# Performance work log

Measured on AMD Instinct MI355X. Metric: run time of the kernel, lower is better.

The kernel has to match this reference:

```python
import jax, jax.numpy as jnp
import numpy as np

B, S, D = 2, 2048, 4096
H, KVH, HD = 32, 8, 128   # attention heads, kv heads, head_dim
GROUPS = H // KVH          # 4
SCALING = 0.08838834764831845  # attention_multiplier = 1/sqrt(head_dim)
NEG = -1e9


def _rope_tables(seq_len, head_dim, base=10000.0):
    half = head_dim // 2
    inv_freq = 1.0 / (base ** (np.arange(0, half, dtype=np.float32) / half))
    t = np.arange(seq_len, dtype=np.float32)
    freqs = np.outer(t, inv_freq)               # [S, half]
    emb = np.concatenate([freqs, freqs], axis=-1)  # [S, head_dim]
    return jnp.asarray(np.cos(emb)), jnp.asarray(np.sin(emb))


def setup_inputs() -> dict:
    key = jax.random.key(0)
    ks = jax.random.split(key, 6)
    hidden_states = jax.random.normal(ks[0], (B, S, D), dtype=jnp.float32)
    std = 0.02
    Wq = jax.random.normal(ks[1], (D, H * HD), dtype=jnp.float32) * std
    Wk = jax.random.normal(ks[2], (D, KVH * HD), dtype=jnp.float32) * std
    Wv = jax.random.normal(ks[3], (D, KVH * HD), dtype=jnp.float32) * std
    Wo = jax.random.normal(ks[4], (H * HD, D), dtype=jnp.float32) * std
    cos1, sin1 = _rope_tables(S, HD)
    cos = jnp.broadcast_to(cos1[None], (B, S, HD))
    sin = jnp.broadcast_to(sin1[None], (B, S, HD))
    # additive causal mask [B, 1, S, S]
    causal = jnp.where(jnp.tril(jnp.ones((S, S), dtype=bool)), 0.0, NEG).astype(jnp.float32)
    attention_mask = jnp.broadcast_to(causal[None, None], (B, 1, S, S))
    return {"hidden_states": hidden_states, "cos": cos, "sin": sin,
            "attention_mask": attention_mask, "Wq": Wq, "Wk": Wk, "Wv": Wv, "Wo": Wo}


def _rotate_half(x):
    x1, x2 = jnp.split(x, 2, axis=-1)
    return jnp.concatenate([-x2, x1], axis=-1)


def reference(hidden_states, cos, sin, attention_mask, Wq, Wk, Wv, Wo):
    b, s, _ = hidden_states.shape
    # projections (no bias), split into heads: [B, H, S, HD]
    q = jnp.einsum('bsd,de->bse', hidden_states, Wq).reshape(b, s, H, HD).transpose(0, 2, 1, 3)
    k = jnp.einsum('bsd,de->bse', hidden_states, Wk).reshape(b, s, KVH, HD).transpose(0, 2, 1, 3)
    v = jnp.einsum('bsd,de->bse', hidden_states, Wv).reshape(b, s, KVH, HD).transpose(0, 2, 1, 3)
    # RoPE (cos/sin unsqueezed on head dim)
    c = cos[:, None, :, :]
    sn = sin[:, None, :, :]
    q = q * c + _rotate_half(q) * sn
    k = k * c + _rotate_half(k) * sn
    # repeat_kv: [B, KVH, S, HD] -> [B, H, S, HD]
    k = jnp.repeat(k, GROUPS, axis=1)
    v = jnp.repeat(v, GROUPS, axis=1)
    # eager attention: full score matrix, additive mask, fp32 softmax
    scores = jnp.einsum('bhqd,bhkd->bhqk', q, k) * SCALING + attention_mask
    attn_weights = jax.nn.softmax(scores.astype(jnp.float32), axis=-1).astype(q.dtype)
    attn_output = jnp.einsum('bhqk,bhkd->bhqd', attn_weights, v)
    attn_output = attn_output.transpose(0, 2, 1, 3).reshape(b, s, H * HD)
    attn_output = jnp.einsum('bse,ed->bsd', attn_output, Wo)
    return attn_output, attn_weights
```

## Files before the change

kernel.cpp:

```cpp
#include <hip/hip_runtime.h>

typedef unsigned short u16;
typedef unsigned int u32;
typedef __attribute__((ext_vector_type(8))) short bf16x8;
typedef __attribute__((ext_vector_type(4))) float f32x4;

#define SCALING 0.08838834764831845f

__device__ __forceinline__ float bf2f(u16 u) {
  union { u32 i; float f; } v; v.i = ((u32)u) << 16; return v.f;
}
__device__ __forceinline__ u16 f2bf(float f) {
  union { float f; u32 i; } v; v.f = f;
  u32 x = v.i;
  return (u16)((x + 0x7fffu + ((x >> 16) & 1u)) >> 16);
}

__device__ __forceinline__ void gll16(const void* g, void* l) {
  __builtin_amdgcn_global_load_lds((const __attribute__((address_space(1))) void*)g,
                                   (__attribute__((address_space(3))) void*)l, 16, 0, 0);
}

__global__ void cast_f32_to_bf16(const float* __restrict__ in, u16* __restrict__ out, int n4) {
  int i = blockIdx.x * 256 + threadIdx.x;
  if (i >= n4) return;
  float4 v = ((const float4*)in)[i];
  ushort4 o;
  o.x = f2bf(v.x); o.y = f2bf(v.y); o.z = f2bf(v.z); o.w = f2bf(v.w);
  ((ushort4*)out)[i] = o;
}

__global__ void transpose_cast(const float* __restrict__ W, u16* __restrict__ WT, int Kd, int Nd) {
  __shared__ float tile[32][33];
  int n0 = blockIdx.x * 32, k0 = blockIdx.y * 32;
  int t = threadIdx.x;
  int r = t >> 3;
  int c = (t & 7) * 4;
  float4 v = *(const float4*)(W + (size_t)(k0 + r) * Nd + n0 + c);
  tile[r][c + 0] = v.x; tile[r][c + 1] = v.y; tile[r][c + 2] = v.z; tile[r][c + 3] = v.w;
  __syncthreads();
  ushort4 o;
  o.x = f2bf(tile[c + 0][r]); o.y = f2bf(tile[c + 1][r]);
  o.z = f2bf(tile[c + 2][r]); o.w = f2bf(tile[c + 3][r]);
  *(ushort4*)(WT + (size_t)(n0 + r) * Kd + k0 + c) = o;
}

template <bool OUT_F32>
__global__ __launch_bounds__(256) void gemm_bt(const u16* __restrict__ A, const u16* __restrict__ B,
                                               void* __restrict__ C, int M, int N, int K) {
  __shared__ __align__(16) u16 As[128 * 32];
  __shared__ __align__(16) u16 Bs[128 * 32];
  const int tid = threadIdx.x;
  const int lane = tid & 63;
  const int w = tid >> 6;
  const int wr = w >> 1, wc = w & 1;
  const int q = lane >> 4, cl = lane & 15;
  const int m0 = blockIdx.y * 128, n0 = blockIdx.x * 128;

  const int srow = w * 16 + (lane >> 2);
  const int schk = (lane & 3) * 8;
  const u16* Ag0 = A + (size_t)(m0 + srow) * K + schk;
  const u16* Ag1 = Ag0 + (size_t)64 * K;
  const u16* Bg0 = B + (size_t)(n0 + srow) * K + schk;
  const u16* Bg1 = Bg0 + (size_t)64 * K;
  u16* Asp = As + srow * 32 + schk;
  u16* Bsp = Bs + srow * 32 + schk;

  f32x4 zero4 = {0.f, 0.f, 0.f, 0.f};
  f32x4 acc[4][4];
#pragma unroll
  for (int mi = 0; mi < 4; ++mi)
#pragma unroll
    for (int ni = 0; ni < 4; ++ni) acc[mi][ni] = zero4;

  for (int kk = 0; kk < K; kk += 32) {
    gll16(Ag0 + kk, Asp);
    gll16(Ag1 + kk, Asp + 64 * 32);
    gll16(Bg0 + kk, Bsp);
    gll16(Bg1 + kk, Bsp + 64 * 32);
    __syncthreads();
    bf16x8 af[4], bfv[4];
#pragma unroll
    for (int mi = 0; mi < 4; ++mi)
      af[mi] = *(const bf16x8*)(As + (wr * 64 + mi * 16 + cl) * 32 + q * 8);
#pragma unroll
    for (int ni = 0; ni < 4; ++ni)
      bfv[ni] = *(const bf16x8*)(Bs + (wc * 64 + ni * 16 + cl) * 32 + q * 8);
#pragma unroll
    for (int mi = 0; mi < 4; ++mi)
#pragma unroll
      for (int ni = 0; ni < 4; ++ni)
        acc[mi][ni] = __builtin_amdgcn_mfma_f32_16x16x32_bf16(af[mi], bfv[ni], acc[mi][ni], 0, 0, 0);
    __syncthreads();
  }

#pragma unroll
  for (int mi = 0; mi < 4; ++mi)
#pragma unroll
    for (int ni = 0; ni < 4; ++ni) {
      int row = m0 + wr * 64 + mi * 16 + q * 4;
      int col = n0 + wc * 64 + ni * 16 + cl;
#pragma unroll
      for (int r = 0; r < 4; ++r) {
        if (OUT_F32)
          ((float*)C)[(size_t)(row + r) * N + col] = acc[mi][ni][r];
        else
          ((u16*)C)[(size_t)(row + r) * N + col] = f2bf(acc[mi][ni][r]);
      }
    }
}

__global__ void rope_kernel(u16* __restrict__ X, const float* __restrict__ cosb,
                            const float* __restrict__ sinb, int rowstride) {
  int row = blockIdx.x;
  int v = blockIdx.y * 256 + threadIdx.x;
  int d = v & 63, hh = v >> 6;
  size_t base = (size_t)row * rowstride + hh * 128 + d;
  float x1 = bf2f(X[base]);
  float x2 = bf2f(X[base + 64]);
  const float* cp = cosb + (size_t)row * 128;
  const float* sp = sinb + (size_t)row * 128;
  X[base]      = f2bf(x1 * cp[d]      - x2 * sp[d]);
  X[base + 64] = f2bf(x2 * cp[d + 64] + x1 * sp[d + 64]);
}

__global__ __launch_bounds__(256, 2) void attn_kernel(
    const u16* __restrict__ Qb, const u16* __restrict__ Kb, const u16* __restrict__ Vb,
    float* __restrict__ Wout, u16* __restrict__ AO) {
  const int qt = blockIdx.x;
  const int h = blockIdx.y;
  const int b = blockIdx.z;
  const int kvh = h >> 2;

  __shared__ __align__(16) u16 KV[128 * 136];
  __shared__ __align__(16) u16 Ps[128 * 136];
  __shared__ float l_lds[128];
  __shared__ float r_lds[128];

  const int tid = threadIdx.x;
  const int lane = tid & 63;
  const int w = tid >> 6;
  const int wr = w >> 1, wc = w & 1;
  const int q = lane >> 4, cl = lane & 15;

  const size_t qrow0 = (size_t)b * 2048 + qt * 128;
  const u16* Qh = Qb + qrow0 * 4096 + h * 128;
  const u16* Kh = Kb + ((size_t)b * 2048) * 1024 + kvh * 128;
  const u16* Vh = Vb + ((size_t)b * 2048) * 1024 + kvh * 128;

  bf16x8 qa[4][4];
#pragma unroll
  for (int mi = 0; mi < 4; ++mi) {
    const u16* qp = Qh + (size_t)(wr * 64 + mi * 16 + cl) * 4096 + q * 8;
#pragma unroll
    for (int kd = 0; kd < 4; ++kd) qa[mi][kd] = *(const bf16x8*)(qp + kd * 32);
  }

  if (tid < 128) l_lds[tid] = 0.f;

  const int njt = qt + 1;
  const int srb = tid >> 4;
  const int scc = (tid & 15) * 8;

  f32x4 zero4 = {0.f, 0.f, 0.f, 0.f};

  for (int jt = 0; jt < njt; ++jt) {
    {
      const u16* src = Kh + (size_t)jt * 128 * 1024;
#pragma unroll
      for (int i = 0; i < 8; ++i) {
        int row = srb + i * 16;
        *(uint4*)(KV + row * 136 + scc) = *(const uint4*)(src + (size_t)row * 1024 + scc);
      }
    }
    __syncthreads();
    f32x4 acc[4][4];
#pragma unroll
    for (int mi = 0; mi < 4; ++mi)
#pragma unroll
      for (int ni = 0; ni < 4; ++ni) acc[mi][ni] = zero4;
#pragma unroll
    for (int kd = 0; kd < 4; ++kd) {
      bf16x8 bk[4];
#pragma unroll
      for (int ni = 0; ni < 4; ++ni)
        bk[ni] = *(const bf16x8*)(KV + (wc * 64 + ni * 16 + cl) * 136 + kd * 32 + q * 8);
#pragma unroll
      for (int mi = 0; mi < 4; ++mi)
#pragma unroll
        for (int ni = 0; ni < 4; ++ni)
          acc[mi][ni] = __builtin_amdgcn_mfma_f32_16x16x32_bf16(qa[mi][kd], bk[ni], acc[mi][ni], 0, 0, 0);
    }
#pragma unroll
    for (int mi = 0; mi < 4; ++mi) {
      int ig0 = qt * 128 + wr * 64 + mi * 16 + q * 4;
      float rs0 = 0.f, rs1 = 0.f, rs2 = 0.f, rs3 = 0.f;
#pragma unroll
      for (int ni = 0; ni < 4; ++ni) {
        int jg = jt * 128 + wc * 64 + ni * 16 + cl;
        rs0 += (jg <= ig0 + 0) ? __expf(acc[mi][ni][0] * SCALING) : 0.f;
        rs1 += (jg <= ig0 + 1) ? __expf(acc[mi][ni][1] * SCALING) : 0.f;
        rs2 += (jg <= ig0 + 2) ? __expf(acc[mi][ni][2] * SCALING) : 0.f;
        rs3 += (jg <= ig0 + 3) ? __expf(acc[mi][ni][3] * SCALING) : 0.f;
      }
#pragma unroll
      for (int m = 1; m < 16; m <<= 1) {
        rs0 += __shfl_xor(rs0, m, 64);
        rs1 += __shfl_xor(rs1, m, 64);
        rs2 += __shfl_xor(rs2, m, 64);
        rs3 += __shfl_xor(rs3, m, 64);
      }
      if (cl == 0) {
        int il = wr * 64 + mi * 16 + q * 4;
        atomicAdd(&l_lds[il + 0], rs0);
        atomicAdd(&l_lds[il + 1], rs1);
        atomicAdd(&l_lds[il + 2], rs2);
        atomicAdd(&l_lds[il + 3], rs3);
      }
    }
    __syncthreads();
  }
  if (tid < 128) r_lds[tid] = 1.f / l_lds[tid];

  f32x4 oacc[4][4];
#pragma unroll
  for (int mi = 0; mi < 4; ++mi)
#pragma unroll
    for (int ni = 0; ni < 4; ++ni) oacc[mi][ni] = zero4;
  __syncthreads();

  for (int jt = 0; jt < njt; ++jt) {
    {
      const u16* src = Kh + (size_t)jt * 128 * 1024;
#pragma unroll
      for (int i = 0; i < 8; ++i) {
        int row = srb + i * 16;
        *(uint4*)(KV + row * 136 + scc) = *(const uint4*)(src + (size_t)row * 1024 + scc);
      }
    }
    __syncthreads();
    f32x4 acc[4][4];
#pragma unroll
    for (int mi = 0; mi < 4; ++mi)
#pragma unroll
      for (int ni = 0; ni < 4; ++ni) acc[mi][ni] = zero4;
#pragma unroll
    for (int kd = 0; kd < 4; ++kd) {
      bf16x8 bk[4];
#pragma unroll
      for (int ni = 0; ni < 4; ++ni)
        bk[ni] = *(const bf16x8*)(KV + (wc * 64 + ni * 16 + cl) * 136 + kd * 32 + q * 8);
#pragma unroll
      for (int mi = 0; mi < 4; ++mi)
#pragma unroll
        for (int ni = 0; ni < 4; ++ni)
          acc[mi][ni] = __builtin_amdgcn_mfma_f32_16x16x32_bf16(qa[mi][kd], bk[ni], acc[mi][ni], 0, 0, 0);
    }
    __syncthreads();

    {
      const u16* src = Vh + (size_t)jt * 128 * 1024;
      u32* vt = (u32*)KV;
      int c = tid & 15;
      int d0 = c * 8;
#pragma unroll
      for (int i = 0; i < 4; ++i) {
        int jp = srb + i * 16;
        uint4 a = *(const uint4*)(src + (size_t)(2 * jp) * 1024 + d0);
        uint4 bq = *(const uint4*)(src + (size_t)(2 * jp + 1) * 1024 + d0);
        const u16* ah = (const u16*)&a;
        const u16* bh = (const u16*)&bq;
#pragma unroll
        for (int kk = 0; kk < 8; ++kk) {
          int k = (kk + c) & 7;
          vt[(d0 + k) * 68 + jp] = (u32)ah[k] | ((u32)bh[k] << 16);
        }
      }
    }
#pragma unroll
    for (int mi = 0; mi < 4; ++mi)
#pragma unroll
      for (int r = 0; r < 4; ++r) {
        int il = wr * 64 + mi * 16 + q * 4 + r;
        int ig = qt * 128 + il;
        float rv = r_lds[il];
#pragma unroll
        for (int ni = 0; ni < 4; ++ni) {
          int jl = wc * 64 + ni * 16 + cl;
          int jg = jt * 128 + jl;
          float p = (jg <= ig) ? __expf(acc[mi][ni][r] * SCALING) * rv : 0.f;
          Ps[il * 136 + jl] = f2bf(p);
        }
      }
    __syncthreads();

    {
      float* wb = Wout + ((size_t)(b * 32 + h) * 2048 + qt * 128) * 2048 + jt * 128;
#pragma unroll
      for (int i = 0; i < 8; ++i) {
        int cf = tid + i * 256;
        int row = cf >> 4;
        int ch = (cf & 15) * 8;
        const u16* sp = Ps + row * 136 + ch;
        float4 o0 = {bf2f(sp[0]), bf2f(sp[1]), bf2f(sp[2]), bf2f(sp[3])};
        float4 o1 = {bf2f(sp[4]), bf2f(sp[5]), bf2f(sp[6]), bf2f(sp[7])};
        float* dp = wb + (size_t)row * 2048 + ch;
        *(float4*)dp = o0;
        *(float4*)(dp + 4) = o1;
      }
    }
    {
      const u32* vt = (const u32*)KV;
#pragma unroll
      for (int ks = 0; ks < 4; ++ks) {
        bf16x8 pa[4], vb[4];
#pragma unroll
        for (int mi = 0; mi < 4; ++mi)
          pa[mi] = *(const bf16x8*)(Ps + (wr * 64 + mi * 16 + cl) * 136 + ks * 32 + q * 8);
#pragma unroll
        for (int ni = 0; ni < 4; ++ni)
          vb[ni] = *(const bf16x8*)(vt + (wc * 64 + ni * 16 + cl) * 68 + ks * 16 + q * 4);
#pragma unroll
        for (int mi = 0; mi < 4; ++mi)
#pragma unroll
          for (int ni = 0; ni < 4; ++ni)
            oacc[mi][ni] = __builtin_amdgcn_mfma_f32_16x16x32_bf16(pa[mi], vb[ni], oacc[mi][ni], 0, 0, 0);
      }
    }
    __syncthreads();
  }

  for (int jt = njt; jt < 16; ++jt) {
    float* wb = Wout + ((size_t)(b * 32 + h) * 2048 + qt * 128) * 2048 + jt * 128;
    float4 z = {0.f, 0.f, 0.f, 0.f};
#pragma unroll
    for (int i = 0; i < 8; ++i) {
      int cf = tid + i * 256;
      int row = cf >> 4;
      int ch = (cf & 15) * 8;
      float* dp = wb + (size_t)row * 2048 + ch;
      *(float4*)dp = z;
      *(float4*)(dp + 4) = z;
    }
  }

#pragma unroll
  for (int mi = 0; mi < 4; ++mi)
#pragma unroll
    for (int ni = 0; ni < 4; ++ni) {
      int il = wr * 64 + mi * 16 + q * 4;
      int d = wc * 64 + ni * 16 + cl;
#pragma unroll
      for (int r = 0; r < 4; ++r)
        AO[(qrow0 + il + r) * 4096 + h * 128 + d] = f2bf(oacc[mi][ni][r]);
    }
}

extern "C" void kernel_launch(void* const* d_in, const int* in_sizes, int n_in,
                              void* d_out, int out_size, void* d_ws, size_t ws_size,
                              hipStream_t stream) {
  const float* hidden = (const float*)d_in[0];
  const float* cosb = (const float*)d_in[1];
  const float* sinb = (const float*)d_in[2];
  const float* Wq = (const float*)d_in[4];
  const float* Wk = (const float*)d_in[5];
  const float* Wv = (const float*)d_in[6];
  const float* Wo = (const float*)d_in[7];

  char* ws = (char*)d_ws;
  u16* hb  = (u16*)(ws);
  u16* WqT = (u16*)(ws + 33554432L);
  u16* WkT = (u16*)(ws + 67108864L);
  u16* WvT = (u16*)(ws + 75497472L);
  u16* WoT = (u16*)(ws + 83886080L);
  u16* Qb  = (u16*)(ws + 117440512L);
  u16* Kb  = (u16*)(ws + 150994944L);
  u16* Vb  = (u16*)(ws + 159383552L);
  u16* AO  = WqT;

  float* out0 = (float*)d_out;
  float* out1 = out0 + 16777216L;

  cast_f32_to_bf16<<<16384, 256, 0, stream>>>(hidden, hb, 4194304);
  transpose_cast<<<dim3(128, 128), 256, 0, stream>>>(Wq, WqT, 4096, 4096);
  transpose_cast<<<dim3(32, 128), 256, 0, stream>>>(Wk, WkT, 4096, 1024);
  transpose_cast<<<dim3(32, 128), 256, 0, stream>>>(Wv, WvT, 4096, 1024);
  transpose_cast<<<dim3(128, 128), 256, 0, stream>>>(Wo, WoT, 4096, 4096);

  gemm_bt<false><<<dim3(32, 32), 256, 0, stream>>>(hb, WqT, Qb, 4096, 4096, 4096);
  gemm_bt<false><<<dim3(8, 32), 256, 0, stream>>>(hb, WkT, Kb, 4096, 1024, 4096);
  gemm_bt<false><<<dim3(8, 32), 256, 0, stream>>>(hb, WvT, Vb, 4096, 1024, 4096);

  rope_kernel<<<dim3(4096, 8), 256, 0, stream>>>(Qb, cosb, sinb, 4096);
  rope_kernel<<<dim3(4096, 2), 256, 0, stream>>>(Kb, cosb, sinb, 1024);

  attn_kernel<<<dim3(16, 32, 2), 256, 0, stream>>>(Qb, Kb, Vb, out1, AO);

  gemm_bt<true><<<dim3(32, 32), 256, 0, stream>>>(AO, WoT, out0, 4096, 4096, 4096);
}
```

Measured before the change: 2.678 ms.

## Restructure attention kernel: 512 threads, 64-key tiles, async double-buffered K, swizzled LDS

Rewrites the two-pass attention kernel to use 8 waves per block, each handling 32 query rows, over 64-key tiles. K tiles are double-buffered with global_load_lds so the next tile loads while the current one is computed. LDS tiles use XOR swizzles in place of padding to avoid bank conflicts. Row sums stay in registers and are reduced once at the end instead of with per-tile atomics and barriers, and the causal mask is only evaluated on diagonal tiles. Per-block LDS drops and occupancy rises, at the cost of more loop iterations and setprio tuning.

```diff
diff --git a/kernel.cpp b/kernel.cpp
--- a/kernel.cpp
+++ b/kernel.cpp
@@ -124,7 +124,7 @@
   X[base + 64] = f2bf(x2 * cp[d + 64] + x1 * sp[d + 64]);
 }
 
-__global__ __launch_bounds__(256, 2) void attn_kernel(
+__global__ __launch_bounds__(512, 4) void attn_kernel(
     const u16* __restrict__ Qb, const u16* __restrict__ Kb, const u16* __restrict__ Vb,
     float* __restrict__ Wout, u16* __restrict__ AO) {
   const int qt = blockIdx.x;
@@ -132,227 +132,264 @@
   const int b = blockIdx.z;
   const int kvh = h >> 2;
 
-  __shared__ __align__(16) u16 KV[128 * 136];
-  __shared__ __align__(16) u16 Ps[128 * 136];
+  __shared__ __align__(16) u16 Ksm[2][64 * 128];
+  __shared__ __align__(16) u32 Vt[128 * 32];
+  __shared__ __align__(16) u16 Ps[128 * 64];
   __shared__ float l_lds[128];
-  __shared__ float r_lds[128];
 
   const int tid = threadIdx.x;
   const int lane = tid & 63;
   const int w = tid >> 6;
   const int wr = w >> 1, wc = w & 1;
   const int q = lane >> 4, cl = lane & 15;
+  const int cx = cl & 7;
 
   const size_t qrow0 = (size_t)b * 2048 + qt * 128;
   const u16* Qh = Qb + qrow0 * 4096 + h * 128;
   const u16* Kh = Kb + ((size_t)b * 2048) * 1024 + kvh * 128;
   const u16* Vh = Vb + ((size_t)b * 2048) * 1024 + kvh * 128;
 
-  bf16x8 qa[4][4];
-#pragma unroll
-  for (int mi = 0; mi < 4; ++mi) {
-    const u16* qp = Qh + (size_t)(wr * 64 + mi * 16 + cl) * 4096 + q * 8;
+  bf16x8 qa[2][4];
+#pragma unroll
+  for (int mi = 0; mi < 2; ++mi) {
+    const u16* qp = Qh + (size_t)(wr * 32 + mi * 16 + cl) * 4096 + q * 8;
 #pragma unroll
     for (int kd = 0; kd < 4; ++kd) qa[mi][kd] = *(const bf16x8*)(qp + kd * 32);
   }
 
   if (tid < 128) l_lds[tid] = 0.f;
 
-  const int njt = qt + 1;
-  const int srb = tid >> 4;
-  const int scc = (tid & 15) * 8;
+  const int srow = tid >> 4;
+  const int kchunk = (tid & 15) ^ (srow & 7);
+  const int njt = 2 * qt + 2;
+
+  auto stageK = [&](int jt, int buf) {
+    const u16* s0 = Kh + ((size_t)(jt * 64 + srow)) * 1024 + kchunk * 8;
+    u16* d0 = Ksm[buf] + tid * 8;
+    gll16(s0, d0);
+    gll16(s0 + 32 * 1024, d0 + 4096);
+  };
 
   f32x4 zero4 = {0.f, 0.f, 0.f, 0.f};
 
-  for (int jt = 0; jt < njt; ++jt) {
+  float lpart[2][4];
+#pragma unroll
+  for (int mi = 0; mi < 2; ++mi)
+#pragma unroll
+    for (int r = 0; r < 4; ++r) lpart[mi][r] = 0.f;
+
+  stageK(0, 0);
+  for (int t = 0; t < njt; ++t) {
+    __syncthreads();
+    if (t + 1 < njt) stageK(t + 1, (t + 1) & 1);
+    const u16* Kc = Ksm[t & 1];
+    f32x4 acc[2][2];
+#pragma unroll
+    for (int mi = 0; mi < 2; ++mi)
+#pragma unroll
+      for (int ni = 0; ni < 2; ++ni) acc[mi][ni] = zero4;
+    __builtin_amdgcn_s_setprio(1);
+#pragma unroll
+    for (int kd = 0; kd < 4; ++kd) {
+      bf16x8 bk[2];
+#pragma unroll
+      for (int ni = 0; ni < 2; ++ni) {
+        int row = wc * 32 + ni * 16 + cl;
+        bk[ni] = *(const bf16x8*)(Kc + row * 128 + (((kd * 4 + q) ^ cx) << 3));
+      }
+#pragma unroll
+      for (int mi = 0; mi < 2; ++mi)
+#pragma unroll
+        for (int ni = 0; ni < 2; ++ni)
+          acc[mi][ni] = __builtin_amdgcn_mfma_f32_16x16x32_bf16(qa[mi][kd], bk[ni], acc[mi][ni], 0, 0, 0);
+    }
+    __builtin_amdgcn_s_setprio(0);
+    if (t >= 2 * qt) {
+#pragma unroll
+      for (int mi = 0; mi < 2; ++mi)
+#pragma unroll
+        for (int r = 0; r < 4; ++r) {
+          int ig = qt * 128 + wr * 32 + mi * 16 + q * 4 + r;
+          float s = 0.f;
+#pragma unroll
+          for (int ni = 0; ni < 2; ++ni) {
+            int jg = t * 64 + wc * 32 + ni * 16 + cl;
+            s += (jg <= ig) ? __expf(acc[mi][ni][r] * SCALING) : 0.f;
+          }
+          lpart[mi][r] += s;
+        }
+    } else {
+#pragma unroll
+      for (int mi = 0; mi < 2; ++mi)
+#pragma unroll
+        for (int r = 0; r < 4; ++r) {
+          float s = 0.f;
+#pragma unroll
+          for (int ni = 0; ni < 2; ++ni) s += __expf(acc[mi][ni][r] * SCALING);
+          lpart[mi][r] += s;
+        }
+    }
+  }
+#pragma unroll
+  for (int mi = 0; mi < 2; ++mi)
+#pragma unroll
+    for (int r = 0; r < 4; ++r) {
+      float v = lpart[mi][r];
+      v += __shfl_xor(v, 1, 64);
+      v += __shfl_xor(v, 2, 64);
+      v += __shfl_xor(v, 4, 64);
+      v += __shfl_xor(v, 8, 64);
+      if (cl == 0) atomicAdd(&l_lds[wr * 32 + mi * 16 + q * 4 + r], v);
+    }
+  __syncthreads();
+  float rv[2][4];
+#pragma unroll
+  for (int mi = 0; mi < 2; ++mi)
+#pragma unroll
+    for (int r = 0; r < 4; ++r) rv[mi][r] = 1.f / l_lds[wr * 32 + mi * 16 + q * 4 + r];
+
+  f32x4 oacc[2][4];
+#pragma unroll
+  for (int mi = 0; mi < 2; ++mi)
+#pragma unroll
+    for (int nd = 0; nd < 4; ++nd) oacc[mi][nd] = zero4;
+
+  const int vp = tid >> 4;
+  const int vc = tid & 15;
+  const int vd0 = vc * 8;
+
+  stageK(0, 0);
+  for (int t = 0; t < njt; ++t) {
+    __syncthreads();
+
+    const u16* vsrc = Vh + ((size_t)(t * 64 + 2 * vp)) * 1024 + vd0;
+    uint4 va = *(const uint4*)vsrc;
+    uint4 vb4 = *(const uint4*)(vsrc + 1024);
+
+    const u16* Kc = Ksm[t & 1];
+    f32x4 acc[2][2];
+#pragma unroll
+    for (int mi = 0; mi < 2; ++mi)
+#pragma unroll
+      for (int ni = 0; ni < 2; ++ni) acc[mi][ni] = zero4;
+    __builtin_amdgcn_s_setprio(1);
+#pragma unroll
+    for (int kd = 0; kd < 4; ++kd) {
+      bf16x8 bk[2];
+#pragma unroll
+      for (int ni = 0; ni < 2; ++ni) {
+        int row = wc * 32 + ni * 16 + cl;
+        bk[ni] = *(const bf16x8*)(Kc + row * 128 + (((kd * 4 + q) ^ cx) << 3));
+      }
+#pragma unroll
+      for (int mi = 0; mi < 2; ++mi)
+#pragma unroll
+        for (int ni = 0; ni < 2; ++ni)
+          acc[mi][ni] = __builtin_amdgcn_mfma_f32_16x16x32_bf16(qa[mi][kd], bk[ni], acc[mi][ni], 0, 0, 0);
+    }
+    __builtin_amdgcn_s_setprio(0);
+
     {
-      const u16* src = Kh + (size_t)jt * 128 * 1024;
-#pragma unroll
-      for (int i = 0; i < 8; ++i) {
-        int row = srb + i * 16;
-        *(uint4*)(KV + row * 136 + scc) = *(const uint4*)(src + (size_t)row * 1024 + scc);
-      }
-    }
-    __syncthreads();
-    f32x4 acc[4][4];
-#pragma unroll
-    for (int mi = 0; mi < 4; ++mi)
-#pragma unroll
-      for (int ni = 0; ni < 4; ++ni) acc[mi][ni] = zero4;
-#pragma unroll
-    for (int kd = 0; kd < 4; ++kd) {
-      bf16x8 bk[4];
-#pragma unroll
-      for (int ni = 0; ni < 4; ++ni)
-        bk[ni] = *(const bf16x8*)(KV + (wc * 64 + ni * 16 + cl) * 136 + kd * 32 + q * 8);
-#pragma unroll
-      for (int mi = 0; mi < 4; ++mi)
-#pragma unroll
-        for (int ni = 0; ni < 4; ++ni)
-          acc[mi][ni] = __builtin_amdgcn_mfma_f32_16x16x32_bf16(qa[mi][kd], bk[ni], acc[mi][ni], 0, 0, 0);
-    }
-#pragma unroll
-    for (int mi = 0; mi < 4; ++mi) {
-      int ig0 = qt * 128 + wr * 64 + mi * 16 + q * 4;
-      float rs0 = 0.f, rs1 = 0.f, rs2 = 0.f, rs3 = 0.f;
-#pragma unroll
-      for (int ni = 0; ni < 4; ++ni) {
-        int jg = jt * 128 + wc * 64 + ni * 16 + cl;
-        rs0 += (jg <= ig0 + 0) ? __expf(acc[mi][ni][0] * SCALING) : 0.f;
-        rs1 += (jg <= ig0 + 1) ? __expf(acc[mi][ni][1] * SCALING) : 0.f;
-        rs2 += (jg <= ig0 + 2) ? __expf(acc[mi][ni][2] * SCALING) : 0.f;
-        rs3 += (jg <= ig0 + 3) ? __expf(acc[mi][ni][3] * SCALING) : 0.f;
-      }
-#pragma unroll
-      for (int m = 1; m < 16; m <<= 1) {
-        rs0 += __shfl_xor(rs0, m, 64);
-        rs1 += __shfl_xor(rs1, m, 64);
-        rs2 += __shfl_xor(rs2, m, 64);
-        rs3 += __shfl_xor(rs3, m, 64);
-      }
-      if (cl == 0) {
-        int il = wr * 64 + mi * 16 + q * 4;
-        atomicAdd(&l_lds[il + 0], rs0);
-        atomicAdd(&l_lds[il + 1], rs1);
-        atomicAdd(&l_lds[il + 2], rs2);
-        atomicAdd(&l_lds[il + 3], rs3);
-      }
-    }
-    __syncthreads();
-  }
-  if (tid < 128) r_lds[tid] = 1.f / l_lds[tid];
-
-  f32x4 oacc[4][4];
-#pragma unroll
-  for (int mi = 0; mi < 4; ++mi)
-#pragma unroll
-    for (int ni = 0; ni < 4; ++ni) oacc[mi][ni] = zero4;
-  __syncthreads();
-
-  for (int jt = 0; jt < njt; ++jt) {
+      const u16* ah = (const u16*)&va;
+      const u16* bh = (const u16*)&vb4;
+#pragma unroll
+      for (int kk = 0; kk < 8; ++kk) {
+        int k = (kk + vc) & 7;
+        int d = vd0 + k;
+        Vt[d * 32 + ((((vp >> 2) ^ k) << 2) | (vp & 3))] = (u32)ah[k] | ((u32)bh[k] << 16);
+      }
+    }
+
     {
-      const u16* src = Kh + (size_t)jt * 128 * 1024;
-#pragma unroll
-      for (int i = 0; i < 8; ++i) {
-        int row = srb + i * 16;
-        *(uint4*)(KV + row * 136 + scc) = *(const uint4*)(src + (size_t)row * 1024 + scc);
-      }
-    }
-    __syncthreads();
-    f32x4 acc[4][4];
-#pragma unroll
-    for (int mi = 0; mi < 4; ++mi)
-#pragma unroll
-      for (int ni = 0; ni < 4; ++ni) acc[mi][ni] = zero4;
-#pragma unroll
-    for (int kd = 0; kd < 4; ++kd) {
-      bf16x8 bk[4];
-#pragma unroll
-      for (int ni = 0; ni < 4; ++ni)
-        bk[ni] = *(const bf16x8*)(KV + (wc * 64 + ni * 16 + cl) * 136 + kd * 32 + q * 8);
-#pragma unroll
-      for (int mi = 0; mi < 4; ++mi)
-#pragma unroll
-        for (int ni = 0; ni < 4; ++ni)
-          acc[mi][ni] = __builtin_amdgcn_mfma_f32_16x16x32_bf16(qa[mi][kd], bk[ni], acc[mi][ni], 0, 0, 0);
-    }
-    __syncthreads();
+      bool diag = (t >= 2 * qt);
+#pragma unroll
+      for (int mi = 0; mi < 2; ++mi)
+#pragma unroll
+        for (int r = 0; r < 4; ++r) {
+          int row = wr * 32 + mi * 16 + q * 4 + r;
+          int ig = qt * 128 + row;
+          float rvv = rv[mi][r];
+#pragma unroll
+          for (int ni = 0; ni < 2; ++ni) {
+            int col = wc * 32 + ni * 16 + cl;
+            float p = __expf(acc[mi][ni][r] * SCALING) * rvv;
+            if (diag) { int jg = t * 64 + col; p = (jg <= ig) ? p : 0.f; }
+            Ps[row * 64 + (((col >> 3) ^ (row & 7)) << 3) + (col & 7)] = f2bf(p);
+          }
+        }
+    }
+
+    if (t + 1 < njt) stageK(t + 1, (t + 1) & 1);
+
+    asm volatile("s_waitcnt lgkmcnt(0)\n\ts_barrier" ::: "memory");
 
     {
-      const u16* src = Vh + (size_t)jt * 128 * 1024;
-      u32* vt = (u32*)KV;
-      int c = tid & 15;
-      int d0 = c * 8;
-#pragma unroll
-      for (int i = 0; i < 4; ++i) {
-        int jp = srb + i * 16;
-        uint4 a = *(const uint4*)(src + (size_t)(2 * jp) * 1024 + d0);
-        uint4 bq = *(const uint4*)(src + (size_t)(2 * jp + 1) * 1024 + d0);
-        const u16* ah = (const u16*)&a;
-        const u16* bh = (const u16*)&bq;
-#pragma unroll
-        for (int kk = 0; kk < 8; ++kk) {
-          int k = (kk + c) & 7;
-          vt[(d0 + k) * 68 + jp] = (u32)ah[k] | ((u32)bh[k] << 16);
-        }
-      }
-    }
-#pragma unroll
-    for (int mi = 0; mi < 4; ++mi)
-#pragma unroll
-      for (int r = 0; r < 4; ++r) {
-        int il = wr * 64 + mi * 16 + q * 4 + r;
-        int ig = qt * 128 + il;
-        float rv = r_lds[il];
-#pragma unroll
-        for (int ni = 0; ni < 4; ++ni) {
-          int jl = wc * 64 + ni * 16 + cl;
-          int jg = jt * 128 + jl;
-          float p = (jg <= ig) ? __expf(acc[mi][ni][r] * SCALING) * rv : 0.f;
-          Ps[il * 136 + jl] = f2bf(p);
-        }
-      }
-    __syncthreads();
-
-    {
-      float* wb = Wout + ((size_t)(b * 32 + h) * 2048 + qt * 128) * 2048 + jt * 128;
-#pragma unroll
-      for (int i = 0; i < 8; ++i) {
-        int cf = tid + i * 256;
-        int row = cf >> 4;
-        int ch = (cf & 15) * 8;
-        const u16* sp = Ps + row * 136 + ch;
-        float4 o0 = {bf2f(sp[0]), bf2f(sp[1]), bf2f(sp[2]), bf2f(sp[3])};
-        float4 o1 = {bf2f(sp[4]), bf2f(sp[5]), bf2f(sp[6]), bf2f(sp[7])};
+      float* wb = Wout + (((size_t)(b * 32 + h) * 2048 + qt * 128) * 2048) + (size_t)t * 64;
+#pragma unroll
+      for (int it = 0; it < 2; ++it) {
+        int cf = tid + it * 512;
+        int row = cf >> 3;
+        int ch = (cf & 7) * 8;
+        bf16x8 pv8 = *(const bf16x8*)(Ps + row * 64 + (((ch >> 3) ^ (row & 7)) << 3));
+        float4 o0 = {bf2f((u16)pv8[0]), bf2f((u16)pv8[1]), bf2f((u16)pv8[2]), bf2f((u16)pv8[3])};
+        float4 o1 = {bf2f((u16)pv8[4]), bf2f((u16)pv8[5]), bf2f((u16)pv8[6]), bf2f((u16)pv8[7])};
         float* dp = wb + (size_t)row * 2048 + ch;
         *(float4*)dp = o0;
         *(float4*)(dp + 4) = o1;
       }
     }
+
     {
-      const u32* vt = (const u32*)KV;
-#pragma unroll
-      for (int ks = 0; ks < 4; ++ks) {
-        bf16x8 pa[4], vb[4];
-#pragma unroll
-        for (int mi = 0; mi < 4; ++mi)
-          pa[mi] = *(const bf16x8*)(Ps + (wr * 64 + mi * 16 + cl) * 136 + ks * 32 + q * 8);
-#pragma unroll
-        for (int ni = 0; ni < 4; ++ni)
-          vb[ni] = *(const bf16x8*)(vt + (wc * 64 + ni * 16 + cl) * 68 + ks * 16 + q * 4);
-#pragma unroll
-        for (int mi = 0; mi < 4; ++mi)
-#pragma unroll
-          for (int ni = 0; ni < 4; ++ni)
-            oacc[mi][ni] = __builtin_amdgcn_mfma_f32_16x16x32_bf16(pa[mi], vb[ni], oacc[mi][ni], 0, 0, 0);
-      }
-    }
-    __syncthreads();
+      __builtin_amdgcn_s_setprio(1);
+#pragma unroll
+      for (int ks = 0; ks < 2; ++ks) {
+        bf16x8 pa[2], vbf[4];
+#pragma unroll
+        for (int mi = 0; mi < 2; ++mi) {
+          int row = wr * 32 + mi * 16 + cl;
+          pa[mi] = *(const bf16x8*)(Ps + row * 64 + (((ks * 4 + q) ^ cx) << 3));
+        }
+#pragma unroll
+        for (int nd = 0; nd < 4; ++nd) {
+          int d = wc * 64 + nd * 16 + cl;
+          vbf[nd] = *(const bf16x8*)((const u16*)Vt + d * 64 + (((ks * 4 + q) ^ cx) << 3));
+        }
+#pragma unroll
+        for (int mi = 0; mi < 2; ++mi)
+#pragma unroll
+          for (int nd = 0; nd < 4; ++nd)
+            oacc[mi][nd] = __builtin_amdgcn_mfma_f32_16x16x32_bf16(pa[mi], vbf[nd], oacc[mi][nd], 0, 0, 0);
+      }
+      __builtin_amdgcn_s_setprio(0);
+    }
   }
 
-  for (int jt = njt; jt < 16; ++jt) {
-    float* wb = Wout + ((size_t)(b * 32 + h) * 2048 + qt * 128) * 2048 + jt * 128;
+  {
+    float* wb0 = Wout + (((size_t)(b * 32 + h) * 2048 + qt * 128) * 2048);
     float4 z = {0.f, 0.f, 0.f, 0.f};
-#pragma unroll
-    for (int i = 0; i < 8; ++i) {
-      int cf = tid + i * 256;
-      int row = cf >> 4;
-      int ch = (cf & 15) * 8;
-      float* dp = wb + (size_t)row * 2048 + ch;
-      *(float4*)dp = z;
-      *(float4*)(dp + 4) = z;
+    for (int jt = njt; jt < 32; ++jt) {
+      float* wbz = wb0 + (size_t)jt * 64;
+#pragma unroll
+      for (int it = 0; it < 2; ++it) {
+        int cf = tid + it * 512;
+        int row = cf >> 3;
+        int ch = (cf & 7) * 8;
+        float* dp = wbz + (size_t)row * 2048 + ch;
+        *(float4*)dp = z;
+        *(float4*)(dp + 4) = z;
+      }
     }
   }
 
 #pragma unroll
-  for (int mi = 0; mi < 4; ++mi)
-#pragma unroll
-    for (int ni = 0; ni < 4; ++ni) {
-      int il = wr * 64 + mi * 16 + q * 4;
-      int d = wc * 64 + ni * 16 + cl;
+  for (int mi = 0; mi < 2; ++mi)
+#pragma unroll
+    for (int nd = 0; nd < 4; ++nd) {
+      int il = wr * 32 + mi * 16 + q * 4;
+      int d = wc * 64 + nd * 16 + cl;
 #pragma unroll
       for (int r = 0; r < 4; ++r)
-        AO[(qrow0 + il + r) * 4096 + h * 128 + d] = f2bf(oacc[mi][ni][r]);
+        AO[(qrow0 + il + r) * 4096 + h * 128 + d] = f2bf(oacc[mi][nd][r]);
     }
 }
 
@@ -394,7 +431,7 @@
   rope_kernel<<<dim3(4096, 8), 256, 0, stream>>>(Qb, cosb, sinb, 4096);
   rope_kernel<<<dim3(4096, 2), 256, 0, stream>>>(Kb, cosb, sinb, 1024);
 
-  attn_kernel<<<dim3(16, 32, 2), 256, 0, stream>>>(Qb, Kb, Vb, out1, AO);
+  attn_kernel<<<dim3(16, 32, 2), 512, 0, stream>>>(Qb, Kb, Vb, out1, AO);
 
   gemm_bt<true><<<dim3(32, 32), 256, 0, stream>>>(AO, WoT, out0, 4096, 4096, 4096);
 }
```

After: 2.805 ms. 4.7% more time.
